# Kernel tuning notes

Measured on AMD Instinct MI355X. Metric: run time of the kernel, lower is better.

Reference implementation:

```python
import jax, jax.numpy as jnp
import numpy as np

B, A, T = 32, 64, 128
N_IN, N_EMB, N_H = 6, 128, 256
E = 2 * N_EMB  # embedding width = 256


def setup_inputs() -> dict:
    key = jax.random.key(0)
    ks = jax.random.split(key, 7)
    s_emb = 1.0 / np.sqrt(N_IN)
    s_l = 1.0 / np.sqrt(N_H)
    return {
        "inputs": jax.random.normal(ks[0], (B, A, T, N_IN), jnp.float32),
        "W_emb": jax.random.uniform(ks[1], (E, N_IN), jnp.float32, -s_emb, s_emb),
        "b_emb": jax.random.uniform(ks[2], (E,), jnp.float32, -s_emb, s_emb),
        "W_ih": jax.random.uniform(ks[3], (4 * N_H, E), jnp.float32, -s_l, s_l),
        "W_hh": jax.random.uniform(ks[4], (4 * N_H, N_H), jnp.float32, -s_l, s_l),
        "b_ih": jax.random.uniform(ks[5], (4 * N_H,), jnp.float32, -s_l, s_l),
        "b_hh": jax.random.uniform(ks[6], (4 * N_H,), jnp.float32, -s_l, s_l),
    }


def reference(inputs, W_emb, b_emb, W_ih, W_hh, b_ih, b_hh):
    b, a, t, _ = inputs.shape
    n = b * a
    h_dim = W_hh.shape[1]
    # [T, B*A, n_in]: time-major, atoms flattened into batch rows (as in LSTMCell.forward)
    xs = jnp.moveaxis(inputs, 2, 0).reshape(t, n, -1)
    # per-timestep Linear embed, then precompute the input projection of the LSTM
    emb = jnp.einsum("tnf,ef->tne", xs, W_emb) + b_emb          # [T, N, 2*n_emb]
    pre = jnp.einsum("tne,ge->tng", emb, W_ih) + b_ih + b_hh    # [T, N, 4*n_h]

    def step(carry, p):
        h, c = carry
        gates = p + h @ W_hh.T                                  # [N, 4*n_h]
        i, f, g, o = jnp.split(gates, 4, axis=-1)               # PyTorch gate order i,f,g,o
        i = jax.nn.sigmoid(i)
        f = jax.nn.sigmoid(f)
        g = jnp.tanh(g)
        o = jax.nn.sigmoid(o)
        c_new = f * c + i * g
        h_new = o * jnp.tanh(c_new)
        return (h_new, c_new), h_new

    h0 = jnp.zeros((n, h_dim), inputs.dtype)
    c0 = jnp.zeros((n, h_dim), inputs.dtype)
    _, hs = jax.lax.scan(step, (h0, c0), pre)                   # hs: [T, N, n_h]
    hs = hs.reshape(t, b, a, h_dim)
    return jnp.transpose(hs, (1, 2, 0, 3))                      # [B, A, T, n_h]
```

## Files before the change

### kernel.cpp

```cpp
#include <hip/hip_runtime.h>
#include <math.h>


#define TT 128
#define NH 256

typedef __attribute__((ext_vector_type(4))) float f32x4;
typedef __attribute__((ext_vector_type(8))) short s16x8;
typedef union { uint4 u4; s16x8 s; unsigned u[4]; } frag_u;

#define OFF_PUB   589824
#define PUB_UNITS 342
#define NUNITS3   (3 * PUB_UNITS)
#define PUB_STRIDE (PUB_UNITS * 16)
#define PUB_BYTES (2 * 256 * PUB_STRIDE)

__device__ __forceinline__ unsigned short f2bf(float x) {
    unsigned u = __float_as_uint(x);
    return (unsigned short)((u + 0x7FFFu + ((u >> 16) & 1u)) >> 16);
}
__device__ __forceinline__ float bf2f(unsigned b) {
    return __uint_as_float(b << 16);
}

template<int PAT>
__device__ __forceinline__ float qswz(float x) {
    return __int_as_float(__builtin_amdgcn_ds_swizzle(__float_as_int(x), PAT));
}

__global__ void prep(const float* __restrict__ W_emb, const float* __restrict__ b_emb,
                     const float* __restrict__ W_ih,  const float* __restrict__ W_hh,
                     const float* __restrict__ b_ih,  const float* __restrict__ b_hh,
                     unsigned short* __restrict__ wsW)
{
    int tid = blockIdx.x * 256 + threadIdx.x;
    if (tid >= 36864) return;
    int l    = tid & 63;
    int fid  = tid >> 6;
    int kt   = fid % 9;
    int cg16 = fid / 9;
    int l16  = l & 15, lg = l >> 4;
    int c    = l16 >> 2, q = l16 & 3;
    int col  = cg16 * 4 + c;
    int grow = q * 256 + col;
    union { unsigned short u16[8]; uint4 v; } pk;
    if (kt < 8) {
        int k0 = kt * 32 + lg * 8;
        const float* src = &W_hh[grow * 256 + k0];
        #pragma unroll
        for (int i = 0; i < 8; ++i) pk.u16[i] = f2bf(src[i]);
    } else {
        #pragma unroll
        for (int i = 0; i < 8; ++i) pk.u16[i] = 0;
        if (lg == 0) {
            float accf[6] = {0.f, 0.f, 0.f, 0.f, 0.f, 0.f};
            float accb = 0.f;
            for (int e = 0; e < 256; ++e) {
                float wv = W_ih[grow * 256 + e];
                accb += wv * b_emb[e];
                #pragma unroll
                for (int f = 0; f < 6; ++f) accf[f] += wv * W_emb[e * 6 + f];
            }
            #pragma unroll
            for (int f = 0; f < 6; ++f) pk.u16[f] = f2bf(accf[f]);
            pk.u16[6] = f2bf(accb + b_ih[grow] + b_hh[grow]);
        }
    }
    *reinterpret_cast<uint4*>(&wsW[(size_t)fid * 512 + l * 8]) = pk.v;
}

__device__ __forceinline__ float sigmoidf_(float x) { return 1.f / (1.f + __expf(-x)); }
__device__ __forceinline__ float tanhf_(float x) {
    float e = __expf(-2.f * fabsf(x));
    float r = (1.f - e) / (1.f + e);
    return copysignf(r, x);
}

__device__ __forceinline__ uint4 ld16_dev(const void* p) {
    uint4 v;
    asm volatile("global_load_dwordx4 %0, %1, off sc0 sc1\n\ts_waitcnt vmcnt(0)"
                 : "=v"(v) : "v"(p) : "memory");
    return v;
}
__device__ __forceinline__ void st4_dev(void* p, unsigned v) {
    asm volatile("global_store_dword %0, %1, off sc0 sc1" :: "v"(p), "v"(v) : "memory");
}

__device__ __forceinline__ void qgather(const f32x4& acc, bool qb0, bool qb1, float X[4]) {
    float g0, g1, g2, g3, x01, x23;
    g0 = qswz<0x8000>(acc[0]); g1 = qswz<0x8000>(acc[1]);
    g2 = qswz<0x8000>(acc[2]); g3 = qswz<0x8000>(acc[3]);
    x01 = qb0 ? g1 : g0; x23 = qb0 ? g3 : g2; X[0] = qb1 ? x23 : x01;
    g0 = qswz<0x8055>(acc[0]); g1 = qswz<0x8055>(acc[1]);
    g2 = qswz<0x8055>(acc[2]); g3 = qswz<0x8055>(acc[3]);
    x01 = qb0 ? g1 : g0; x23 = qb0 ? g3 : g2; X[1] = qb1 ? x23 : x01;
    g0 = qswz<0x80AA>(acc[0]); g1 = qswz<0x80AA>(acc[1]);
    g2 = qswz<0x80AA>(acc[2]); g3 = qswz<0x80AA>(acc[3]);
    x01 = qb0 ? g1 : g0; x23 = qb0 ? g3 : g2; X[2] = qb1 ? x23 : x01;
    g0 = qswz<0x80FF>(acc[0]); g1 = qswz<0x80FF>(acc[1]);
    g2 = qswz<0x80FF>(acc[2]); g3 = qswz<0x80FF>(acc[3]);
    x01 = qb0 ? g1 : g0; x23 = qb0 ? g3 : g2; X[3] = qb1 ? x23 : x01;
}

__global__ __launch_bounds__(1024, 4)
void lstm_main(const float* __restrict__ xin, const unsigned short* __restrict__ wsW,
               float* __restrict__ out, char* __restrict__ pub)
{
    __shared__ __align__(16) unsigned short hsh[2][32][264];

    const int tid = threadIdx.x;
    const int w   = tid >> 6, l = tid & 63;
    const int l16 = l & 15,  lg = l >> 4;
    const int c   = l16 >> 2, q = l16 & 3;
    const bool qb0 = (q & 1), qb1 = (q & 2);
    const int bid = blockIdx.x;
    const int q4  = bid >> 6;
    const int g   = bid & 63;
    const int n0  = g * 32;
    const int j   = q4 * 64 + w * 4 + c;
    const int cg16 = q4 * 16 + w;

    frag_u Wf[9];
    #pragma unroll
    for (int kt = 0; kt < 9; ++kt) {
        const unsigned short* p = &wsW[(size_t)(cg16 * 9 + kt) * 512 + l * 8];
        asm volatile("global_load_dwordx4 %0, %1, off" : "=v"(Wf[kt].u4) : "v"(p));
    }
    asm volatile("s_waitcnt vmcnt(0)" ::: "memory");

    float cm0 = 0.f, cm1 = 0.f;

    const int iuA = tid;
    const int iuB = tid + 1024;
    const int pA_ord = iuA / PUB_UNITS, uA = iuA - pA_ord * PUB_UNITS;
    const int pB_ord = iuB / PUB_UNITS, uB = iuB - pB_ord * PUB_UNITS;
    const int pA = pA_ord + (pA_ord >= q4 ? 1 : 0);
    const int pB = pB_ord + (pB_ord >= q4 ? 1 : 0);

    for (int t = 0; t < TT; ++t) {
        const int want = t - 1;
        const int pw = want & 1;
        const int cw = t & 1;
        uint4 vA = make_uint4(0u, 0u, 0u, 0u);
        uint4 vB = make_uint4(0u, 0u, 0u, (unsigned)want);
        const char* srcA = nullptr; const char* srcB = nullptr;

        if (t > 0) {
            const char* base = pub + (size_t)pw * 256 * PUB_STRIDE;
            srcA = base + (size_t)(g + 64 * pA) * PUB_STRIDE + uA * 16;
            asm volatile("global_load_dwordx4 %0, %1, off sc0 sc1"
                         : "=v"(vA) : "v"(srcA) : "memory");
            if (iuB < NUNITS3) {
                srcB = base + (size_t)(g + 64 * pB) * PUB_STRIDE + uB * 16;
                asm volatile("global_load_dwordx4 %0, %1, off sc0 sc1"
                             : "=v"(vB) : "v"(srcB) : "memory");
            }
        }

        frag_u xa0, xa1;
        xa0.u4 = (uint4){0u, 0u, 0u, 0u};
        xa1.u4 = (uint4){0u, 0u, 0u, 0u};
        if (lg == 0) {
            union { unsigned short u16[8]; uint4 v; } pk;
            const float* xp0 = xin + ((size_t)(n0 + l16) * TT + t) * 6;
            #pragma unroll
            for (int f = 0; f < 6; ++f) pk.u16[f] = f2bf(xp0[f]);
            pk.u16[6] = 0x3F80; pk.u16[7] = 0;
            xa0.u4 = pk.v;
            const float* xp1 = xin + ((size_t)(n0 + 16 + l16) * TT + t) * 6;
            #pragma unroll
            for (int f = 0; f < 6; ++f) pk.u16[f] = f2bf(xp1[f]);
            pk.u16[6] = 0x3F80; pk.u16[7] = 0;
            xa1.u4 = pk.v;
        }

        if (t > 0) {
            asm volatile("s_waitcnt vmcnt(0)" ::: "memory");
            __builtin_amdgcn_sched_barrier(0);
            bool okA = ((int)vA.w == want);
            bool okB = (iuB >= NUNITS3) || ((int)vB.w == want);
            int it = 0;
            while (__ballot(!(okA && okB)) != 0ull) {
                __builtin_amdgcn_s_sleep(1);
                if (!okA) { vA = ld16_dev(srcA); okA = ((int)vA.w == want); }
                if (!okB) { vB = ld16_dev(srcB); okB = ((int)vB.w == want); }
                if (++it > (1 << 13)) break;
            }
            {
                const int D0 = 3 * uA;
                {   int r = D0 >> 5, d = D0 & 31;
                    *reinterpret_cast<unsigned*>(&hsh[pw][r][pA * 64 + 2 * d]) = vA.x; }
                if (D0 + 1 < 1024) { int r = (D0 + 1) >> 5, d = (D0 + 1) & 31;
                    *reinterpret_cast<unsigned*>(&hsh[pw][r][pA * 64 + 2 * d]) = vA.y; }
                if (D0 + 2 < 1024) { int r = (D0 + 2) >> 5, d = (D0 + 2) & 31;
                    *reinterpret_cast<unsigned*>(&hsh[pw][r][pA * 64 + 2 * d]) = vA.z; }
            }
            if (iuB < NUNITS3) {
                const int D0 = 3 * uB;
                {   int r = D0 >> 5, d = D0 & 31;
                    *reinterpret_cast<unsigned*>(&hsh[pw][r][pB * 64 + 2 * d]) = vB.x; }
                if (D0 + 1 < 1024) { int r = (D0 + 1) >> 5, d = (D0 + 1) & 31;
                    *reinterpret_cast<unsigned*>(&hsh[pw][r][pB * 64 + 2 * d]) = vB.y; }
                if (D0 + 2 < 1024) { int r = (D0 + 2) >> 5, d = (D0 + 2) & 31;
                    *reinterpret_cast<unsigned*>(&hsh[pw][r][pB * 64 + 2 * d]) = vB.z; }
            }
        }
        __syncthreads();

        f32x4 acc0 = (f32x4){0.f, 0.f, 0.f, 0.f};
        f32x4 acc1 = (f32x4){0.f, 0.f, 0.f, 0.f};
        if (t > 0) {
            #pragma unroll
            for (int kt = 0; kt < 8; ++kt) {
                s16x8 a0 = *reinterpret_cast<const s16x8*>(&hsh[pw][l16     ][kt * 32 + lg * 8]);
                s16x8 a1 = *reinterpret_cast<const s16x8*>(&hsh[pw][16 + l16][kt * 32 + lg * 8]);
                acc0 = __builtin_amdgcn_mfma_f32_16x16x32_bf16(a0, Wf[kt].s, acc0, 0, 0, 0);
                acc1 = __builtin_amdgcn_mfma_f32_16x16x32_bf16(a1, Wf[kt].s, acc1, 0, 0, 0);
            }
        }
        acc0 = __builtin_amdgcn_mfma_f32_16x16x32_bf16(xa0.s, Wf[8].s, acc0, 0, 0, 0);
        acc1 = __builtin_amdgcn_mfma_f32_16x16x32_bf16(xa1.s, Wf[8].s, acc1, 0, 0, 0);

        float hn0, hn1;
        {
            float X[4];
            qgather(acc0, qb0, qb1, X);
            float cn = fmaf(sigmoidf_(X[1]), cm0, sigmoidf_(X[0]) * tanhf_(X[2]));
            cm0 = cn;
            hn0 = sigmoidf_(X[3]) * tanhf_(cn);
            qgather(acc1, qb0, qb1, X);
            cn = fmaf(sigmoidf_(X[1]), cm1, sigmoidf_(X[0]) * tanhf_(X[2]));
            cm1 = cn;
            hn1 = sigmoidf_(X[3]) * tanhf_(cn);
        }
        hsh[cw][lg * 4 + q     ][j] = f2bf(hn0);
        hsh[cw][16 + lg * 4 + q][j] = f2bf(hn1);
        __syncthreads();

        char* dst = nullptr;
        if (t < TT - 1 && tid < PUB_UNITS) {
            const int u = tid, D0 = 3 * u;
            unsigned px, py = 0, pz = 0;
            { int r = D0 >> 5, d = D0 & 31;
              px = *reinterpret_cast<const unsigned*>(&hsh[cw][r][q4 * 64 + 2 * d]); }
            if (D0 + 1 < 1024) { int r = (D0 + 1) >> 5, d = (D0 + 1) & 31;
              py = *reinterpret_cast<const unsigned*>(&hsh[cw][r][q4 * 64 + 2 * d]); }
            if (D0 + 2 < 1024) { int r = (D0 + 2) >> 5, d = (D0 + 2) & 31;
              pz = *reinterpret_cast<const unsigned*>(&hsh[cw][r][q4 * 64 + 2 * d]); }
            dst = pub + ((size_t)cw * 256 + bid) * PUB_STRIDE + u * 16;
            st4_dev(dst,     px);
            st4_dev(dst + 4, py);
            st4_dev(dst + 8, pz);
        }
        asm volatile("s_waitcnt vmcnt(0)" ::: "memory");
        if (t < TT - 1 && tid < PUB_UNITS)
            st4_dev(dst + 12, (unsigned)t);

        {
            int r = tid >> 5, d = tid & 31;
            unsigned hv = *reinterpret_cast<const unsigned*>(&hsh[cw][r][q4 * 64 + 2 * d]);
            float2 ov = make_float2(bf2f(hv & 0xffffu), bf2f(hv >> 16));
            *reinterpret_cast<float2*>(
                &out[((size_t)(n0 + r) * TT + t) * NH + q4 * 64 + 2 * d]) = ov;
        }
    }
}

extern "C" void kernel_launch(void* const* d_in, const int* in_sizes, int n_in,
                              void* d_out, int out_size, void* d_ws, size_t ws_size,
                              hipStream_t stream)
{
    const float* xin   = (const float*)d_in[0];
    const float* W_emb = (const float*)d_in[1];
    const float* b_emb = (const float*)d_in[2];
    const float* W_ih  = (const float*)d_in[3];
    const float* W_hh  = (const float*)d_in[4];
    const float* b_ih  = (const float*)d_in[5];
    const float* b_hh  = (const float*)d_in[6];
    float* out = (float*)d_out;

    unsigned short* wsW = (unsigned short*)d_ws;
    char* pub = (char*)d_ws + OFF_PUB;

    (void)hipMemsetAsync(pub, 0xFF, PUB_BYTES, stream);
    prep<<<144, 256, 0, stream>>>(W_emb, b_emb, W_ih, W_hh, b_ih, b_hh, wsW);
    lstm_main<<<256, 1024, 0, stream>>>(xin, wsW, out, pub);
}
```

Baseline: 907.2 us.

## Publish hidden state directly from registers with per-dword tags, drop second barrier

Each h-value pair now carries its own timestep tag in a dwordx2 record, so the producer writes straight from registers after a lane swizzle instead of staging through shared memory. That removes the second __syncthreads and the store-wait-then-tag sequence. Consumers fetch three 8-byte tagged records per thread instead of packed 16-byte units. The output is also written from registers in fp32 rather than bf16-rounded values re-read from LDS. In exchange the publish buffer grows and polling uses more, smaller loads.

```diff
diff --git a/kernel.cpp b/kernel.cpp
--- a/kernel.cpp
+++ b/kernel.cpp
@@ -9,11 +9,9 @@
 typedef __attribute__((ext_vector_type(8))) short s16x8;
 typedef union { uint4 u4; s16x8 s; unsigned u[4]; } frag_u;
 
-#define OFF_PUB   589824
-#define PUB_UNITS 342
-#define NUNITS3   (3 * PUB_UNITS)
-#define PUB_STRIDE (PUB_UNITS * 16)
-#define PUB_BYTES (2 * 256 * PUB_STRIDE)
+#define OFF_PUB    589824
+#define PUB_STRIDE 8192
+#define PUB_BYTES  (2 * 256 * PUB_STRIDE)
 
 __device__ __forceinline__ unsigned short f2bf(float x) {
     unsigned u = __float_as_uint(x);
@@ -76,14 +74,14 @@
     return copysignf(r, x);
 }
 
-__device__ __forceinline__ uint4 ld16_dev(const void* p) {
-    uint4 v;
-    asm volatile("global_load_dwordx4 %0, %1, off sc0 sc1\n\ts_waitcnt vmcnt(0)"
+__device__ __forceinline__ unsigned long long ld8_dev(const void* p) {
+    unsigned long long v;
+    asm volatile("global_load_dwordx2 %0, %1, off sc0 sc1\n\ts_waitcnt vmcnt(0)"
                  : "=v"(v) : "v"(p) : "memory");
     return v;
 }
-__device__ __forceinline__ void st4_dev(void* p, unsigned v) {
-    asm volatile("global_store_dword %0, %1, off sc0 sc1" :: "v"(p), "v"(v) : "memory");
+__device__ __forceinline__ void st8_dev(void* p, unsigned long long v) {
+    asm volatile("global_store_dwordx2 %0, %1, off sc0 sc1" :: "v"(p), "v"(v) : "memory");
 }
 
 __device__ __forceinline__ void qgather(const f32x4& acc, bool qb0, bool qb1, float X[4]) {
@@ -119,6 +117,9 @@
     const int n0  = g * 32;
     const int j   = q4 * 64 + w * 4 + c;
     const int cg16 = q4 * 16 + w;
+    const int R0  = lg * 4 + q;
+    const int R1  = 16 + R0;
+    const bool evc = ((c & 1) == 0);
 
     frag_u Wf[9];
     #pragma unroll
@@ -130,31 +131,29 @@
 
     float cm0 = 0.f, cm1 = 0.f;
 
-    const int iuA = tid;
-    const int iuB = tid + 1024;
-    const int pA_ord = iuA / PUB_UNITS, uA = iuA - pA_ord * PUB_UNITS;
-    const int pB_ord = iuB / PUB_UNITS, uB = iuB - pB_ord * PUB_UNITS;
-    const int pA = pA_ord + (pA_ord >= q4 ? 1 : 0);
-    const int pB = pB_ord + (pB_ord >= q4 ? 1 : 0);
+    const int pp0 = 0 + (0 >= q4);
+    const int pp1 = pp0 + 1 + (pp0 + 1 == q4);
+    const int pp2 = pp1 + 1 + (pp1 + 1 == q4);
+    const int sr  = tid >> 5;
+    const int sd  = tid & 31;
+    const int updx = w * 2 + (c >> 1);
 
     for (int t = 0; t < TT; ++t) {
         const int want = t - 1;
+        const unsigned wtag = (unsigned)want;
         const int pw = want & 1;
         const int cw = t & 1;
-        uint4 vA = make_uint4(0u, 0u, 0u, 0u);
-        uint4 vB = make_uint4(0u, 0u, 0u, (unsigned)want);
-        const char* srcA = nullptr; const char* srcB = nullptr;
+        unsigned long long v0 = 0, v1 = 0, v2 = 0;
+        const char *s0 = nullptr, *s1 = nullptr, *s2 = nullptr;
 
         if (t > 0) {
-            const char* base = pub + (size_t)pw * 256 * PUB_STRIDE;
-            srcA = base + (size_t)(g + 64 * pA) * PUB_STRIDE + uA * 16;
-            asm volatile("global_load_dwordx4 %0, %1, off sc0 sc1"
-                         : "=v"(vA) : "v"(srcA) : "memory");
-            if (iuB < NUNITS3) {
-                srcB = base + (size_t)(g + 64 * pB) * PUB_STRIDE + uB * 16;
-                asm volatile("global_load_dwordx4 %0, %1, off sc0 sc1"
-                             : "=v"(vB) : "v"(srcB) : "memory");
-            }
+            const char* base = pub + (size_t)pw * 256 * PUB_STRIDE + (size_t)tid * 8;
+            s0 = base + (size_t)(g + 64 * pp0) * PUB_STRIDE;
+            s1 = base + (size_t)(g + 64 * pp1) * PUB_STRIDE;
+            s2 = base + (size_t)(g + 64 * pp2) * PUB_STRIDE;
+            asm volatile("global_load_dwordx2 %0, %1, off sc0 sc1" : "=v"(v0) : "v"(s0) : "memory");
+            asm volatile("global_load_dwordx2 %0, %1, off sc0 sc1" : "=v"(v1) : "v"(s1) : "memory");
+            asm volatile("global_load_dwordx2 %0, %1, off sc0 sc1" : "=v"(v2) : "v"(s2) : "memory");
         }
 
         frag_u xa0, xa1;
@@ -177,33 +176,20 @@
         if (t > 0) {
             asm volatile("s_waitcnt vmcnt(0)" ::: "memory");
             __builtin_amdgcn_sched_barrier(0);
-            bool okA = ((int)vA.w == want);
-            bool okB = (iuB >= NUNITS3) || ((int)vB.w == want);
+            bool ok0 = ((unsigned)(v0 >> 32) == wtag);
+            bool ok1 = ((unsigned)(v1 >> 32) == wtag);
+            bool ok2 = ((unsigned)(v2 >> 32) == wtag);
             int it = 0;
-            while (__ballot(!(okA && okB)) != 0ull) {
+            while (__ballot(!(ok0 && ok1 && ok2)) != 0ull) {
                 __builtin_amdgcn_s_sleep(1);
-                if (!okA) { vA = ld16_dev(srcA); okA = ((int)vA.w == want); }
-                if (!okB) { vB = ld16_dev(srcB); okB = ((int)vB.w == want); }
-                if (++it > (1 << 13)) break;
-            }
-            {
-                const int D0 = 3 * uA;
-                {   int r = D0 >> 5, d = D0 & 31;
-                    *reinterpret_cast<unsigned*>(&hsh[pw][r][pA * 64 + 2 * d]) = vA.x; }
-                if (D0 + 1 < 1024) { int r = (D0 + 1) >> 5, d = (D0 + 1) & 31;
-                    *reinterpret_cast<unsigned*>(&hsh[pw][r][pA * 64 + 2 * d]) = vA.y; }
-                if (D0 + 2 < 1024) { int r = (D0 + 2) >> 5, d = (D0 + 2) & 31;
-                    *reinterpret_cast<unsigned*>(&hsh[pw][r][pA * 64 + 2 * d]) = vA.z; }
-            }
-            if (iuB < NUNITS3) {
-                const int D0 = 3 * uB;
-                {   int r = D0 >> 5, d = D0 & 31;
-                    *reinterpret_cast<unsigned*>(&hsh[pw][r][pB * 64 + 2 * d]) = vB.x; }
-                if (D0 + 1 < 1024) { int r = (D0 + 1) >> 5, d = (D0 + 1) & 31;
-                    *reinterpret_cast<unsigned*>(&hsh[pw][r][pB * 64 + 2 * d]) = vB.y; }
-                if (D0 + 2 < 1024) { int r = (D0 + 2) >> 5, d = (D0 + 2) & 31;
-                    *reinterpret_cast<unsigned*>(&hsh[pw][r][pB * 64 + 2 * d]) = vB.z; }
-            }
+                if (!ok0) { v0 = ld8_dev(s0); ok0 = ((unsigned)(v0 >> 32) == wtag); }
+                if (!ok1) { v1 = ld8_dev(s1); ok1 = ((unsigned)(v1 >> 32) == wtag); }
+                if (!ok2) { v2 = ld8_dev(s2); ok2 = ((unsigned)(v2 >> 32) == wtag); }
+                if (++it > (1 << 14)) break;
+            }
+            *reinterpret_cast<unsigned*>(&hsh[pw][sr][pp0 * 64 + 2 * sd]) = (unsigned)v0;
+            *reinterpret_cast<unsigned*>(&hsh[pw][sr][pp1 * 64 + 2 * sd]) = (unsigned)v1;
+            *reinterpret_cast<unsigned*>(&hsh[pw][sr][pp2 * 64 + 2 * sd]) = (unsigned)v2;
         }
         __syncthreads();
 
@@ -233,35 +219,25 @@
             cm1 = cn;
             hn1 = sigmoidf_(X[3]) * tanhf_(cn);
         }
-        hsh[cw][lg * 4 + q     ][j] = f2bf(hn0);
-        hsh[cw][16 + lg * 4 + q][j] = f2bf(hn1);
-        __syncthreads();
-
-        char* dst = nullptr;
-        if (t < TT - 1 && tid < PUB_UNITS) {
-            const int u = tid, D0 = 3 * u;
-            unsigned px, py = 0, pz = 0;
-            { int r = D0 >> 5, d = D0 & 31;
-              px = *reinterpret_cast<const unsigned*>(&hsh[cw][r][q4 * 64 + 2 * d]); }
-            if (D0 + 1 < 1024) { int r = (D0 + 1) >> 5, d = (D0 + 1) & 31;
-              py = *reinterpret_cast<const unsigned*>(&hsh[cw][r][q4 * 64 + 2 * d]); }
-            if (D0 + 2 < 1024) { int r = (D0 + 2) >> 5, d = (D0 + 2) & 31;
-              pz = *reinterpret_cast<const unsigned*>(&hsh[cw][r][q4 * 64 + 2 * d]); }
-            dst = pub + ((size_t)cw * 256 + bid) * PUB_STRIDE + u * 16;
-            st4_dev(dst,     px);
-            st4_dev(dst + 4, py);
-            st4_dev(dst + 8, pz);
-        }
-        asm volatile("s_waitcnt vmcnt(0)" ::: "memory");
-        if (t < TT - 1 && tid < PUB_UNITS)
-            st4_dev(dst + 12, (unsigned)t);
-
-        {
-            int r = tid >> 5, d = tid & 31;
-            unsigned hv = *reinterpret_cast<const unsigned*>(&hsh[cw][r][q4 * 64 + 2 * d]);
-            float2 ov = make_float2(bf2f(hv & 0xffffu), bf2f(hv >> 16));
-            *reinterpret_cast<float2*>(
-                &out[((size_t)(n0 + r) * TT + t) * NH + q4 * 64 + 2 * d]) = ov;
+        const unsigned us0 = f2bf(hn0), us1 = f2bf(hn1);
+        hsh[cw][R0][j] = (unsigned short)us0;
+        hsh[cw][R1][j] = (unsigned short)us1;
+
+        float hp0 = qswz<0x101F>(hn0);
+        float hp1 = qswz<0x101F>(hn1);
+        if (evc) {
+            if (t < TT - 1) {
+                const unsigned long long tagbits = ((unsigned long long)(unsigned)t) << 32;
+                unsigned d0 = (us0 & 0xffffu) | ((unsigned)f2bf(hp0) << 16);
+                unsigned d1 = (us1 & 0xffffu) | ((unsigned)f2bf(hp1) << 16);
+                char* dstb = pub + ((size_t)cw * 256 + bid) * PUB_STRIDE;
+                st8_dev(dstb + (size_t)(R0 * 32 + updx) * 8, (unsigned long long)d0 | tagbits);
+                st8_dev(dstb + (size_t)(R1 * 32 + updx) * 8, (unsigned long long)d1 | tagbits);
+            }
+            *reinterpret_cast<float2*>(&out[((size_t)(n0 + R0) * TT + t) * NH + j])
+                = make_float2(hn0, hp0);
+            *reinterpret_cast<float2*>(&out[((size_t)(n0 + R1) * TT + t) * NH + j])
+                = make_float2(hn1, hp1);
         }
     }
 }
```

Result: slower. 1.407 ms (+55.1%).
